# Kernel tuning notes

Measured on AMD Instinct MI355X. Metric: run time of the kernel, lower is better.

The kernel has to match this reference:

```python
import jax, jax.numpy as jnp
import numpy as np

IN_F = 4096
OUT_F = 4096
GROUP_SIZE = 128
BITS = 4
N_GROUPS = IN_F // GROUP_SIZE  # 32
PACK = 32 // BITS  # 8 nibbles per int32


def setup_inputs() -> dict:
    key = jax.random.key(0)
    k0, k1, k2, k3, k4, k5 = jax.random.split(key, 6)
    x = jax.random.normal(k0, (4, 2048, IN_F), dtype=jnp.float32)
    qweight = jax.random.randint(k1, (IN_F // 32 * BITS, OUT_F), 0, 2**31 - 1, dtype=jnp.int32)
    qzeros = jax.random.randint(k2, (N_GROUPS, OUT_F // 32 * BITS), 0, 2**31 - 1, dtype=jnp.int32)
    # per-group weight scales (already divided by int8_scales*2**(8-bits) at pack time)
    scales = jax.random.uniform(k3, (N_GROUPS, OUT_F), jnp.float32, 0.5, 1.5) * 0.01
    int8_scales = jax.random.uniform(k4, (1, OUT_F), jnp.float32, 0.5, 1.5) * 0.02
    bias = jax.random.normal(k5, (OUT_F,), dtype=jnp.float32) * 0.01
    g_idx = (jnp.arange(IN_F, dtype=jnp.int32) // GROUP_SIZE).astype(jnp.int32)
    return {"x": x, "qweight": qweight, "qzeros": qzeros, "scales": scales,
            "int8_scales": int8_scales, "bias": bias, "g_idx": g_idx}


def reference(x, qweight, qzeros, scales, int8_scales, bias, g_idx):
    wf = jnp.arange(0, 32, BITS, dtype=jnp.int32)  # [8] nibble shift amounts
    # Unpack zero points: [G, out//8] -> [G, out//8, 8] -> int8 (<<4 wraps mod 256) -> [G, out]
    zeros = ((((qzeros[:, :, None] >> wf[None, None, :]) & 15) << 4)
             .astype(jnp.int8).reshape(scales.shape))
    # Unpack weights: [in//8, out] -> [in//8, 8, out] -> [in, out] int8 (values are nibble<<4, wrapped)
    weight = ((((qweight[:, None, :] >> wf[None, :, None]) & 15) << 4)
              .astype(jnp.int8).reshape(IN_F, OUT_F))
    # group_size != infeatures branch: rescale to int8 weights
    diff = weight - zeros[g_idx]  # int8 modular arithmetic, matching torch
    weights = jnp.clip(jnp.round(scales[g_idx] * diff.astype(jnp.float32)),
                       -128, 127).astype(jnp.int8)  # [in, out]
    # dynamic per-token activation quantization
    out_shape = x.shape[:-1] + (OUT_F,)
    xs = x.reshape(-1, IN_F)
    x_scales = (jnp.max(jnp.abs(xs), axis=-1, keepdims=True) / 127.0).astype(jnp.float32)  # [N,1]
    quant_x = jnp.clip(jnp.round(xs / x_scales), -128, 127).astype(jnp.int8)  # [N,in]
    acc = jax.lax.dot_general(quant_x, weights, (((1,), (0,)), ((), ())),
                              preferred_element_type=jnp.int32)  # [N,out]
    dequant = x_scales * int8_scales.astype(jnp.float32)  # [N,out] via broadcast
    out = acc.astype(jnp.float32) * dequant + bias
    return out.reshape(out_shape)
```

## Files before the change

kernel.cpp:

```cpp
#include <hip/hip_runtime.h>
#include <stdint.h>

#define IN_F 4096
#define OUT_F 4096
#define NTOK 8192
#define BM 128
#define BN 128
#define BK 64

typedef int int4v __attribute__((ext_vector_type(4)));

typedef const __attribute__((address_space(1))) void* gas1_t;
typedef __attribute__((address_space(3))) void* gas3_t;

__device__ __forceinline__ void gload_lds16(const int8_t* g, int8_t* l) {
  __builtin_amdgcn_global_load_lds((gas1_t)(const void*)g, (gas3_t)(void*)l, 16, 0, 0);
}

__global__ __launch_bounds__(256) void act_quant_kernel(
    const float* __restrict__ x, int8_t* __restrict__ xq, float* __restrict__ xs)
{
  const int row = blockIdx.x;
  const int t = threadIdx.x;
  const float* xr = x + (size_t)row * IN_F;
  float4 v[4];
  float amax = 0.f;
#pragma unroll
  for (int i = 0; i < 4; ++i) {
    v[i] = reinterpret_cast<const float4*>(xr)[t * 4 + i];
    amax = fmaxf(amax, fmaxf(fmaxf(fabsf(v[i].x), fabsf(v[i].y)),
                             fmaxf(fabsf(v[i].z), fabsf(v[i].w))));
  }
#pragma unroll
  for (int off = 32; off; off >>= 1)
    amax = fmaxf(amax, __shfl_xor(amax, off));
  __shared__ float red[4];
  if ((t & 63) == 0) red[t >> 6] = amax;
  __syncthreads();
  amax = fmaxf(fmaxf(red[0], red[1]), fmaxf(red[2], red[3]));
  const float s = amax / 127.0f;
  if (t == 0) xs[row] = s;

  int4v packed;
#pragma unroll
  for (int i = 0; i < 4; ++i) {
    int q0 = (int)rintf(v[i].x / s);
    int q1 = (int)rintf(v[i].y / s);
    int q2 = (int)rintf(v[i].z / s);
    int q3 = (int)rintf(v[i].w / s);
    q0 = max(-128, min(127, q0));
    q1 = max(-128, min(127, q1));
    q2 = max(-128, min(127, q2));
    q3 = max(-128, min(127, q3));
    packed[i] = (q0 & 255) | ((q1 & 255) << 8) | ((q2 & 255) << 16) | (q3 << 24);
  }
  *reinterpret_cast<int4v*>(xq + (size_t)row * IN_F + t * 16) = packed;
}

__global__ __launch_bounds__(256) void wdq_kernel(
    const int* __restrict__ qweight, const int* __restrict__ qzeros,
    const float* __restrict__ scales, int8_t* __restrict__ wt)
{
  __shared__ int8_t tile[64 * 144];
  const int t = threadIdx.x;
  const int g = blockIdx.x;
  const int o0 = blockIdx.y * 64;
  const int i0 = g * 16;
  const int ol = t & 63;
  const int o = o0 + ol;

  const int zw = qzeros[g * (OUT_F / 8) + (o >> 3)];
  const int znib = (zw >> ((o & 7) * 4)) & 15;
  const float sc = scales[g * OUT_F + o];

#pragma unroll
  for (int j = 0; j < 4; ++j) {
    const int il = j * 4 + (t >> 6);
    const int w = qweight[(size_t)(i0 + il) * OUT_F + o];
    uint64_t packed = 0;
#pragma unroll
    for (int nb = 0; nb < 8; ++nb) {
      const int wnib = (w >> (nb * 4)) & 15;
      const int8_t diff = (int8_t)(((wnib - znib) & 15) << 4);
      float val = rintf(sc * (float)diff);
      val = fminf(127.f, fmaxf(-128.f, val));
      packed |= (uint64_t)(uint8_t)(int8_t)(int)val << (8 * nb);
    }
    *reinterpret_cast<uint64_t*>(&tile[ol * 144 + il * 8]) = packed;
  }
  __syncthreads();
  const int orow = t >> 2;
  const int kb = (t & 3) * 32;
  int4v w0 = *reinterpret_cast<int4v*>(&tile[orow * 144 + kb]);
  int4v w1 = *reinterpret_cast<int4v*>(&tile[orow * 144 + kb + 16]);
  int8_t* dst = wt + (size_t)(o0 + orow) * IN_F + g * 128 + kb;
  *reinterpret_cast<int4v*>(dst) = w0;
  *reinterpret_cast<int4v*>(dst + 16) = w1;
}

__global__ __launch_bounds__(256) void gemm_kernel(
    const int8_t* __restrict__ aq, const int8_t* __restrict__ wt,
    const float* __restrict__ xs, const float* __restrict__ int8_scales,
    const float* __restrict__ bias, float* __restrict__ out)
{
  __shared__ int8_t a_lds[BM * BK];
  __shared__ int8_t b_lds[BN * BK];

  int bid = blockIdx.x;
  const int cpx = gridDim.x >> 3;
  bid = (bid & 7) * cpx + (bid >> 3);
  const int mtile = bid >> 5;
  const int ntile = bid & 31;
  const int m0 = mtile * BM;
  const int n0 = ntile * BN;

  const int t = threadIdx.x;
  const int l = t & 63;
  const int w = t >> 6;
  const int wm = (w >> 1) * 64;
  const int wn = (w & 1) * 64;

  const int lrow = t >> 2;
  const int lbyte = (t & 3) * 16;
  const int8_t* a_src = aq + (size_t)(m0 + lrow) * IN_F + lbyte;
  const int8_t* b_src = wt + (size_t)(n0 + lrow) * IN_F + lbyte;
  int8_t* a_dst = a_lds + t * 16;
  int8_t* b_dst = b_lds + t * 16;

  int4v acc[4][4];
#pragma unroll
  for (int i = 0; i < 4; ++i)
#pragma unroll
    for (int j = 0; j < 4; ++j)
      acc[i][j] = (int4v){0, 0, 0, 0};

  const int4v* a_fp = reinterpret_cast<const int4v*>(a_lds) + (wm + (l & 15)) * 4 + (l >> 4);
  const int4v* b_fp = reinterpret_cast<const int4v*>(b_lds) + (wn + (l & 15)) * 4 + (l >> 4);

  for (int kt = 0; kt < IN_F / BK; ++kt) {
    const int koff = kt * BK;
    gload_lds16(a_src + koff, a_dst);
    gload_lds16(a_src + (size_t)64 * IN_F + koff, a_dst + 4096);
    gload_lds16(b_src + koff, b_dst);
    gload_lds16(b_src + (size_t)64 * IN_F + koff, b_dst + 4096);
    __syncthreads();

    int4v af[4], bf[4];
#pragma unroll
    for (int i = 0; i < 4; ++i) af[i] = a_fp[i * 64];
#pragma unroll
    for (int j = 0; j < 4; ++j) bf[j] = b_fp[j * 64];
#pragma unroll
    for (int i = 0; i < 4; ++i)
#pragma unroll
      for (int j = 0; j < 4; ++j)
        acc[i][j] = __builtin_amdgcn_mfma_i32_16x16x64_i8(af[i], bf[j], acc[i][j], 0, 0, 0);
    __syncthreads();
  }

  float xsv[4][4];
#pragma unroll
  for (int mf = 0; mf < 4; ++mf)
#pragma unroll
    for (int r = 0; r < 4; ++r)
      xsv[mf][r] = xs[m0 + wm + mf * 16 + (l >> 4) * 4 + r];

#pragma unroll
  for (int nf = 0; nf < 4; ++nf) {
    const int col = n0 + wn + nf * 16 + (l & 15);
    const float is = int8_scales[col];
    const float bv = bias[col];
#pragma unroll
    for (int mf = 0; mf < 4; ++mf) {
      const int rowb = m0 + wm + mf * 16 + (l >> 4) * 4;
#pragma unroll
      for (int r = 0; r < 4; ++r) {
        const float dq = xsv[mf][r] * is;
        out[(size_t)(rowb + r) * OUT_F + col] = (float)acc[mf][nf][r] * dq + bv;
      }
    }
  }
}

extern "C" void kernel_launch(void* const* d_in, const int* in_sizes, int n_in,
                              void* d_out, int out_size, void* d_ws, size_t ws_size,
                              hipStream_t stream) {
  const float* x           = (const float*)d_in[0];
  const int*   qweight     = (const int*)d_in[1];
  const int*   qzeros      = (const int*)d_in[2];
  const float* scales      = (const float*)d_in[3];
  const float* int8_scales = (const float*)d_in[4];
  const float* bias        = (const float*)d_in[5];
  float* out = (float*)d_out;

  int8_t* aq = (int8_t*)d_ws;
  int8_t* wt = aq + (size_t)NTOK * IN_F;
  float*  xs = (float*)(wt + (size_t)OUT_F * IN_F);

  act_quant_kernel<<<NTOK, 256, 0, stream>>>(x, aq, xs);
  wdq_kernel<<<dim3(IN_F / 128, OUT_F / 64), 256, 0, stream>>>(qweight, qzeros, scales, wt);
  gemm_kernel<<<(NTOK / BM) * (OUT_F / BN), 256, 0, stream>>>(aq, wt, xs, int8_scales, bias, out);
}
```

Baseline: 417.9 us.

## Rewrite int8 GEMM with 256x256 tiles, 4-stage LDS pipeline and swizzle

The GEMM moves to 256x256 block tiles with 512 threads and a four-buffer LDS ring filled by direct global-to-LDS loads three tiles ahead. Explicit vmcnt waits with one barrier per k-step replace the two syncthreads per iteration. An XOR swizzle on the LDS layout is meant to avoid bank conflicts, and s_setprio raises priority around the MFMA block. The activation quant kernel switches to coalesced strided accesses. The cost is 128KB of dynamic LDS and more accumulator registers per thread, which limits occupancy, and the hand-written inline-asm synchronisation is fragile.

```diff
diff --git a/kernel.cpp b/kernel.cpp
--- a/kernel.cpp
+++ b/kernel.cpp
@@ -4,9 +4,10 @@
 #define IN_F 4096
 #define OUT_F 4096
 #define NTOK 8192
-#define BM 128
-#define BN 128
+#define BM 256
+#define BN 256
 #define BK 64
+#define NKT (IN_F / BK)
 
 typedef int int4v __attribute__((ext_vector_type(4)));
 
@@ -22,12 +23,12 @@
 {
   const int row = blockIdx.x;
   const int t = threadIdx.x;
-  const float* xr = x + (size_t)row * IN_F;
+  const float4* xr = reinterpret_cast<const float4*>(x + (size_t)row * IN_F);
   float4 v[4];
   float amax = 0.f;
 #pragma unroll
   for (int i = 0; i < 4; ++i) {
-    v[i] = reinterpret_cast<const float4*>(xr)[t * 4 + i];
+    v[i] = xr[t + i * 256];
     amax = fmaxf(amax, fmaxf(fmaxf(fabsf(v[i].x), fabsf(v[i].y)),
                              fmaxf(fabsf(v[i].z), fabsf(v[i].w))));
   }
@@ -41,7 +42,7 @@
   const float s = amax / 127.0f;
   if (t == 0) xs[row] = s;
 
-  int4v packed;
+  uint32_t* xqw = reinterpret_cast<uint32_t*>(xq + (size_t)row * IN_F);
 #pragma unroll
   for (int i = 0; i < 4; ++i) {
     int q0 = (int)rintf(v[i].x / s);
@@ -52,9 +53,8 @@
     q1 = max(-128, min(127, q1));
     q2 = max(-128, min(127, q2));
     q3 = max(-128, min(127, q3));
-    packed[i] = (q0 & 255) | ((q1 & 255) << 8) | ((q2 & 255) << 16) | (q3 << 24);
-  }
-  *reinterpret_cast<int4v*>(xq + (size_t)row * IN_F + t * 16) = packed;
+    xqw[t + i * 256] = (q0 & 255) | ((q1 & 255) << 8) | ((q2 & 255) << 16) | (q3 << 24);
+  }
 }
 
 __global__ __launch_bounds__(256) void wdq_kernel(
@@ -98,86 +98,132 @@
   *reinterpret_cast<int4v*>(dst + 16) = w1;
 }
 
-__global__ __launch_bounds__(256) void gemm_kernel(
+extern __shared__ int8_t g_lds[];
+
+template<int BUF, int VM, bool STG>
+__device__ __forceinline__ void tile_step(
+    int kt,
+    const int8_t*& pa, const int8_t*& pb,
+    const int8_t*& psa, const int8_t*& psb,
+    int8_t* lds_st, int4v (&acc)[8][4])
+{
+  if constexpr (VM == 8)
+    asm volatile("s_waitcnt vmcnt(8)\n\ts_barrier"
+                 : "+v"(pa), "+v"(pb), "+v"(psa), "+v"(psb) :: "memory");
+  else if constexpr (VM == 4)
+    asm volatile("s_waitcnt vmcnt(4)\n\ts_barrier"
+                 : "+v"(pa), "+v"(pb), "+v"(psa), "+v"(psb) :: "memory");
+  else
+    asm volatile("s_waitcnt vmcnt(0)\n\ts_barrier"
+                 : "+v"(pa), "+v"(pb), "+v"(psa), "+v"(psb) :: "memory");
+
+  int4v af[8], bf[4];
+#pragma unroll
+  for (int mf = 0; mf < 8; ++mf)
+    af[mf] = *reinterpret_cast<const int4v*>(pa + BUF * 16384 + mf * 1024);
+#pragma unroll
+  for (int nf = 0; nf < 4; ++nf)
+    bf[nf] = *reinterpret_cast<const int4v*>(pb + BUF * 16384 + nf * 1024);
+
+  if constexpr (STG) {
+    const int8_t* as = psa + (kt + 3) * BK;
+    const int8_t* bs = psb + (kt + 3) * BK;
+    int8_t* ad = lds_st + ((BUF + 3) & 3) * 16384;
+    int8_t* bd = ad + 65536;
+    gload_lds16(as, ad);
+    gload_lds16(as + 128 * IN_F, ad + 8192);
+    gload_lds16(bs, bd);
+    gload_lds16(bs + 128 * IN_F, bd + 8192);
+  }
+
+  __builtin_amdgcn_s_setprio(1);
+#pragma unroll
+  for (int mf = 0; mf < 8; ++mf)
+#pragma unroll
+    for (int nf = 0; nf < 4; ++nf)
+      acc[mf][nf] = __builtin_amdgcn_mfma_i32_16x16x64_i8(af[mf], bf[nf],
+                                                          acc[mf][nf], 0, 0, 0);
+  __builtin_amdgcn_s_setprio(0);
+}
+
+__global__ __launch_bounds__(512, 2) void gemm_kernel(
     const int8_t* __restrict__ aq, const int8_t* __restrict__ wt,
     const float* __restrict__ xs, const float* __restrict__ int8_scales,
     const float* __restrict__ bias, float* __restrict__ out)
 {
-  __shared__ int8_t a_lds[BM * BK];
-  __shared__ int8_t b_lds[BN * BK];
-
   int bid = blockIdx.x;
-  const int cpx = gridDim.x >> 3;
-  bid = (bid & 7) * cpx + (bid >> 3);
-  const int mtile = bid >> 5;
-  const int ntile = bid & 31;
-  const int m0 = mtile * BM;
-  const int n0 = ntile * BN;
+  bid = (bid & 7) * 64 + (bid >> 3);
+  const int m0 = (bid >> 4) * BM;
+  const int n0 = (bid & 15) * BN;
 
   const int t = threadIdx.x;
   const int l = t & 63;
   const int w = t >> 6;
-  const int wm = (w >> 1) * 64;
-  const int wn = (w & 1) * 64;
-
-  const int lrow = t >> 2;
-  const int lbyte = (t & 3) * 16;
-  const int8_t* a_src = aq + (size_t)(m0 + lrow) * IN_F + lbyte;
-  const int8_t* b_src = wt + (size_t)(n0 + lrow) * IN_F + lbyte;
-  int8_t* a_dst = a_lds + t * 16;
-  int8_t* b_dst = b_lds + t * 16;
-
-  int4v acc[4][4];
-#pragma unroll
-  for (int i = 0; i < 4; ++i)
-#pragma unroll
-    for (int j = 0; j < 4; ++j)
-      acc[i][j] = (int4v){0, 0, 0, 0};
-
-  const int4v* a_fp = reinterpret_cast<const int4v*>(a_lds) + (wm + (l & 15)) * 4 + (l >> 4);
-  const int4v* b_fp = reinterpret_cast<const int4v*>(b_lds) + (wn + (l & 15)) * 4 + (l >> 4);
-
-  for (int kt = 0; kt < IN_F / BK; ++kt) {
-    const int koff = kt * BK;
-    gload_lds16(a_src + koff, a_dst);
-    gload_lds16(a_src + (size_t)64 * IN_F + koff, a_dst + 4096);
-    gload_lds16(b_src + koff, b_dst);
-    gload_lds16(b_src + (size_t)64 * IN_F + koff, b_dst + 4096);
-    __syncthreads();
-
-    int4v af[4], bf[4];
-#pragma unroll
-    for (int i = 0; i < 4; ++i) af[i] = a_fp[i * 64];
-#pragma unroll
-    for (int j = 0; j < 4; ++j) bf[j] = b_fp[j * 64];
-#pragma unroll
-    for (int i = 0; i < 4; ++i)
-#pragma unroll
-      for (int j = 0; j < 4; ++j)
-        acc[i][j] = __builtin_amdgcn_mfma_i32_16x16x64_i8(af[i], bf[j], acc[i][j], 0, 0, 0);
-    __syncthreads();
-  }
-
-  float xsv[4][4];
-#pragma unroll
-  for (int mf = 0; mf < 4; ++mf)
+  const int wm = (w >> 2) * 128;
+  const int wn = (w & 3) * 64;
+
+  const int scol = (((t & 3) ^ ((t >> 3) & 3)) << 4);
+  const int8_t* psa = aq + (size_t)(m0 + (t >> 2)) * IN_F + scol;
+  const int8_t* psb = wt + (size_t)(n0 + (t >> 2)) * IN_F + scol;
+  int8_t* lds_st = g_lds + t * 16;
+
+  const int kslot = l >> 4;
+  const int swz = (((l & 15) >> 1) & 3) << 4;
+  const int8_t* pa = g_lds + (wm + (l & 15)) * 64 + ((kslot << 4) ^ swz);
+  const int8_t* pb = g_lds + 65536 + (wn + (l & 15)) * 64 + ((kslot << 4) ^ swz);
+
+  int4v acc[8][4];
+#pragma unroll
+  for (int mf = 0; mf < 8; ++mf)
+#pragma unroll
+    for (int nf = 0; nf < 4; ++nf)
+      acc[mf][nf] = (int4v){0, 0, 0, 0};
+
+#pragma unroll
+  for (int pt = 0; pt < 3; ++pt) {
+    const int8_t* as = psa + pt * BK;
+    const int8_t* bs = psb + pt * BK;
+    int8_t* ad = lds_st + pt * 16384;
+    int8_t* bd = ad + 65536;
+    gload_lds16(as, ad);
+    gload_lds16(as + 128 * IN_F, ad + 8192);
+    gload_lds16(bs, bd);
+    gload_lds16(bs + 128 * IN_F, bd + 8192);
+  }
+
+#pragma unroll 1
+  for (int kt = 0; kt < 60; kt += 4) {
+    tile_step<0, 8, true>(kt + 0, pa, pb, psa, psb, lds_st, acc);
+    tile_step<1, 8, true>(kt + 1, pa, pb, psa, psb, lds_st, acc);
+    tile_step<2, 8, true>(kt + 2, pa, pb, psa, psb, lds_st, acc);
+    tile_step<3, 8, true>(kt + 3, pa, pb, psa, psb, lds_st, acc);
+  }
+  tile_step<0, 8, true >(60, pa, pb, psa, psb, lds_st, acc);
+  tile_step<1, 8, false>(61, pa, pb, psa, psb, lds_st, acc);
+  tile_step<2, 4, false>(62, pa, pb, psa, psb, lds_st, acc);
+  tile_step<3, 0, false>(63, pa, pb, psa, psb, lds_st, acc);
+
+  const int col_l = l & 15;
+  const int row_l = (l >> 4) * 4;
+  float xsv[8][4];
+#pragma unroll
+  for (int mf = 0; mf < 8; ++mf)
 #pragma unroll
     for (int r = 0; r < 4; ++r)
-      xsv[mf][r] = xs[m0 + wm + mf * 16 + (l >> 4) * 4 + r];
+      xsv[mf][r] = xs[m0 + wm + mf * 16 + row_l + r];
 
 #pragma unroll
   for (int nf = 0; nf < 4; ++nf) {
-    const int col = n0 + wn + nf * 16 + (l & 15);
+    const int col = n0 + wn + nf * 16 + col_l;
     const float is = int8_scales[col];
     const float bv = bias[col];
 #pragma unroll
-    for (int mf = 0; mf < 4; ++mf) {
-      const int rowb = m0 + wm + mf * 16 + (l >> 4) * 4;
-#pragma unroll
-      for (int r = 0; r < 4; ++r) {
-        const float dq = xsv[mf][r] * is;
-        out[(size_t)(rowb + r) * OUT_F + col] = (float)acc[mf][nf][r] * dq + bv;
-      }
+    for (int mf = 0; mf < 8; ++mf) {
+      const int rowb = m0 + wm + mf * 16 + row_l;
+#pragma unroll
+      for (int r = 0; r < 4; ++r)
+        out[(size_t)(rowb + r) * OUT_F + col] =
+            (float)acc[mf][nf][r] * (xsv[mf][r] * is) + bv;
     }
   }
 }
@@ -197,7 +243,10 @@
   int8_t* wt = aq + (size_t)NTOK * IN_F;
   float*  xs = (float*)(wt + (size_t)OUT_F * IN_F);
 
+  (void)hipFuncSetAttribute((const void*)gemm_kernel,
+                            hipFuncAttributeMaxDynamicSharedMemorySize, 131072);
+
   act_quant_kernel<<<NTOK, 256, 0, stream>>>(x, aq, xs);
   wdq_kernel<<<dim3(IN_F / 128, OUT_F / 64), 256, 0, stream>>>(qweight, qzeros, scales, wt);
-  gemm_kernel<<<(NTOK / BM) * (OUT_F / BN), 256, 0, stream>>>(aq, wt, xs, int8_scales, bias, out);
-}
+  gemm_kernel<<<(NTOK / BM) * (OUT_F / BN), 512, 131072, stream>>>(aq, wt, xs, int8_scales, bias, out);
+}
```

Measured after the change: 451.1 us. 8.0% more time.
